# Kernel tuning notes

Hardware: AMD Instinct MI355X
Metric: run time of the kernel (lower is better)

The kernel has to match this reference:

```python
import jax, jax.numpy as jnp
import numpy as np

NUM_STUDENTS = 50000
NUM_PROBLEMS = 10000
EMBED_DIM = 64
NNZ = 3200000


def _spmm(rows, cols, vals, x, num_out):
    # out[r] = sum_{edges e with rows[e]==r} vals[e] * x[cols[e]]
    msgs = vals[:, None] * x[cols]  # [nnz, d]
    return jax.ops.segment_sum(msgs, rows, num_segments=num_out)


def setup_inputs() -> dict:
    key = jax.random.key(0)
    ks = jax.random.split(key, 8)
    return {
        "student_embeds": jax.random.normal(ks[0], (NUM_STUDENTS, EMBED_DIM), jnp.float32),
        "problem_embeds": jax.random.normal(ks[1], (NUM_PROBLEMS, EMBED_DIM), jnp.float32),
        "a_rows": jax.random.randint(ks[2], (NNZ,), 0, NUM_STUDENTS, jnp.int32),
        "a_cols": jax.random.randint(ks[3], (NNZ,), 0, NUM_PROBLEMS, jnp.int32),
        "a_vals": jax.random.uniform(ks[4], (NNZ,), jnp.float32),
        "ia_rows": jax.random.randint(ks[5], (NNZ,), 0, NUM_STUDENTS, jnp.int32),
        "ia_cols": jax.random.randint(ks[6], (NNZ,), 0, NUM_PROBLEMS, jnp.int32),
        "ia_vals": jax.random.uniform(ks[7], (NNZ,), jnp.float32),
    }


def reference(student_embeds, problem_embeds, a_rows, a_cols, a_vals,
              ia_rows, ia_cols, ia_vals):
    num_students = student_embeds.shape[0]
    num_problems = problem_embeds.shape[0]
    # a_matrix @ problem_embeds
    student_embeds_c = _spmm(a_rows, a_cols, a_vals, problem_embeds, num_students)
    # a_matrix.T @ student_embeds (swap roles of rows/cols)
    problem_embeds_c = _spmm(a_cols, a_rows, a_vals, student_embeds, num_problems)
    student_embeds_ic = _spmm(ia_rows, ia_cols, ia_vals, problem_embeds, num_students)
    problem_embeds_ic = _spmm(ia_cols, ia_rows, ia_vals, student_embeds, num_problems)
    return (student_embeds_c, student_embeds_ic, problem_embeds_c, problem_embeds_ic)
```

## Files before the change

### kernel.cpp

```cpp
#include <hip/hip_runtime.h>
#include <hip/hip_bf16.h>

#define NBMAX 256
#define TILE  4096
#define KPT   16
#define FTILE 2048
#define FKPT  8
#define BINSMAX 512

__device__ __forceinline__ int seg8(unsigned r, unsigned mult8) {
    return (int)__umulhi(r, mult8);
}

__global__ __launch_bounds__(256) void hist_all(
        const int* __restrict__ k0, const int* __restrict__ k1,
        const int* __restrict__ k2, const int* __restrict__ k3,
        int* __restrict__ gcnt4, int nnz, int rsh_s, int rsh_p) {
    __shared__ int h[NBMAX];
    int dir = blockIdx.x & 3;
    const int* key = (dir == 0) ? k0 : (dir == 1) ? k1 : (dir == 2) ? k2 : k3;
    int rsh = (dir & 1) ? rsh_p : rsh_s;
    h[threadIdx.x] = 0;
    __syncthreads();
    int ch = blockIdx.x >> 2, nch = gridDim.x >> 2;
    int nnz4 = nnz >> 2;
    for (int i = ch * 256 + threadIdx.x; i < nnz4; i += nch * 256) {
        int4 k4 = ((const int4*)key)[i];
        atomicAdd(&h[k4.x >> rsh], 1);
        atomicAdd(&h[k4.y >> rsh], 1);
        atomicAdd(&h[k4.z >> rsh], 1);
        atomicAdd(&h[k4.w >> rsh], 1);
    }
    if (ch == 0) {
        for (int i = (nnz4 << 2) + threadIdx.x; i < nnz; i += 256)
            atomicAdd(&h[key[i] >> rsh], 1);
    }
    __syncthreads();
    int v = h[threadIdx.x];
    if (v) atomicAdd(&gcnt4[dir * NBMAX + threadIdx.x], v);
}

__global__ __launch_bounds__(256) void scan_all(
        const int* __restrict__ gcnt4, int* __restrict__ boffs4,
        int* __restrict__ bcur4, int nb_s, int nb_p, int nnz,
        int* __restrict__ offsE, int* __restrict__ offsO, int NS, int NP8) {
    __shared__ int tmp[NBMAX];
    int dir = blockIdx.x, tid = threadIdx.x;
    int nb = (dir & 1) ? nb_p : nb_s;
    int v = (tid < nb) ? gcnt4[dir * NBMAX + tid] : 0;
    tmp[tid] = v;
    __syncthreads();
    for (int off = 1; off < NBMAX; off <<= 1) {
        int t = (tid >= off) ? tmp[tid - off] : 0;
        __syncthreads();
        tmp[tid] += t;
        __syncthreads();
    }
    if (tid < nb) {
        int e = tmp[tid] - v;
        boffs4[dir * (NBMAX + 1) + tid] = e;
        bcur4[dir * NBMAX + tid] = e;
    }
    if (tid == 0) boffs4[dir * (NBMAX + 1) + nb] = nnz;
    if (dir == 0 && tid == 0) { offsE[NS] = nnz; offsO[NP8] = nnz; }
}

__global__ __launch_bounds__(256) void staged_scatter(
        const int* __restrict__ key, const int* __restrict__ other,
        const float* __restrict__ vals, int* __restrict__ cursor,
        uint2* __restrict__ edges, int nnz, int rsh) {
    __shared__ int lhist[NBMAX], lofs[NBMAX], lbase[NBMAX];
    __shared__ uint2 stage[TILE];
    __shared__ int   sslot[TILE];
    int tid = threadIdx.x;
    int lmask = (1 << rsh) - 1;
    int ntiles = (nnz + TILE - 1) / TILE;
    for (int tile = blockIdx.x; tile < ntiles; tile += gridDim.x) {
        int tbeg = tile * TILE;
        int n = nnz - tbeg; if (n > TILE) n = TILE;
        lhist[tid] = 0;
        __syncthreads();
        int myb[KPT], myr[KPT]; unsigned myo[KPT]; float myv[KPT];
        #pragma unroll
        for (int g = 0; g < 4; ++g) {
            int s = g * 1024 + tid * 4;
            if (s + 4 <= n) {
                int i = tbeg + s;
                int4   k4 = *(const int4*)(key + i);
                int4   o4 = *(const int4*)(other + i);
                float4 v4 = *(const float4*)(vals + i);
                int   kk[4] = {k4.x, k4.y, k4.z, k4.w};
                int   oo[4] = {o4.x, o4.y, o4.z, o4.w};
                float vv[4] = {v4.x, v4.y, v4.z, v4.w};
                #pragma unroll
                for (int k = 0; k < 4; ++k) {
                    int m = g * 4 + k;
                    myb[m] = kk[k] >> rsh;
                    myo[m] = (unsigned)oo[k] | ((unsigned)(kk[k] & lmask) << 16);
                    myv[m] = vv[k];
                    myr[m] = atomicAdd(&lhist[myb[m]], 1);
                }
            } else {
                #pragma unroll
                for (int k = 0; k < 4; ++k) {
                    int m = g * 4 + k;
                    int s2 = s + k;
                    if (s2 < n) {
                        int i = tbeg + s2;
                        int ky = key[i];
                        myb[m] = ky >> rsh;
                        myo[m] = (unsigned)other[i] | ((unsigned)(ky & lmask) << 16);
                        myv[m] = vals[i];
                        myr[m] = atomicAdd(&lhist[myb[m]], 1);
                    } else myb[m] = -1;
                }
            }
        }
        __syncthreads();
        int h = lhist[tid];
        lofs[tid] = h;
        __syncthreads();
        for (int off = 1; off < NBMAX; off <<= 1) {
            int t = (tid >= off) ? lofs[tid - off] : 0;
            __syncthreads();
            lofs[tid] += t;
            __syncthreads();
        }
        lofs[tid] -= h;
        if (h > 0) lbase[tid] = atomicAdd(&cursor[tid], h);
        __syncthreads();
        #pragma unroll
        for (int k = 0; k < KPT; ++k) {
            if (myb[k] >= 0) {
                int ls = lofs[myb[k]] + myr[k];
                stage[ls] = make_uint2(myo[k], __float_as_uint(myv[k]));
                sslot[ls] = lbase[myb[k]] + myr[k];
            }
        }
        __syncthreads();
        #pragma unroll
        for (int k = 0; k < KPT; ++k) {
            int s = k * 256 + tid;
            if (s < n) edges[sslot[s]] = stage[s];
        }
        __syncthreads();
    }
}

__global__ __launch_bounds__(256) void staged_scatter2(
        const int* __restrict__ krow, const int* __restrict__ kcol,
        const float* __restrict__ vals,
        int* __restrict__ curE, int* __restrict__ curO,
        uint2* __restrict__ edgesE, uint2* __restrict__ edgesO,
        int nnz, int rsh_e, int rsh_o, int sgrid,
        const float* __restrict__ rpart, float* __restrict__ rout, int n4red) {
    __shared__ int lhistE[NBMAX], lofsE[NBMAX], lbaseE[NBMAX];
    __shared__ int lhistO[NBMAX], lofsO[NBMAX], lbaseO[NBMAX];
    __shared__ uint2 stageE[FTILE], stageO[FTILE];
    __shared__ int   sslotE[FTILE], sslotO[FTILE];
    int tid = threadIdx.x;
    int nred = (n4red + 255) >> 8;
    if ((int)blockIdx.x < nred) {
        int i = blockIdx.x * 256 + tid;
        if (i < n4red) {
            const float4* p = (const float4*)rpart;
            float4 s = make_float4(0.f, 0.f, 0.f, 0.f);
            #pragma unroll
            for (int xx = 0; xx < 8; ++xx) {
                float4 v = p[(size_t)xx * n4red + i];
                s.x += v.x; s.y += v.y; s.z += v.z; s.w += v.w;
            }
            ((float4*)rout)[i] = s;
        }
        return;
    }
    int sb = blockIdx.x - nred;
    int lmE = (1 << rsh_e) - 1, lmO = (1 << rsh_o) - 1;
    int ntiles = (nnz + FTILE - 1) / FTILE;
    for (int tile = sb; tile < ntiles; tile += sgrid) {
        int tbeg = tile * FTILE;
        int n = nnz - tbeg; if (n > FTILE) n = FTILE;
        lhistE[tid] = 0; lhistO[tid] = 0;
        __syncthreads();
        int mbE[FKPT], mrE[FKPT]; unsigned moE[FKPT];
        int mbO[FKPT], mrO[FKPT]; unsigned moO[FKPT];
        float mv[FKPT];
        #pragma unroll
        for (int g = 0; g < 2; ++g) {
            int s = g * 1024 + tid * 4;
            if (s + 4 <= n) {
                int i = tbeg + s;
                int4   r4 = *(const int4*)(krow + i);
                int4   c4 = *(const int4*)(kcol + i);
                float4 v4 = *(const float4*)(vals + i);
                int   rr[4] = {r4.x, r4.y, r4.z, r4.w};
                int   cc[4] = {c4.x, c4.y, c4.z, c4.w};
                float vv[4] = {v4.x, v4.y, v4.z, v4.w};
                #pragma unroll
                for (int k = 0; k < 4; ++k) {
                    int m = g * 4 + k;
                    mv[m]  = vv[k];
                    mbE[m] = rr[k] >> rsh_e;
                    moE[m] = (unsigned)cc[k] | ((unsigned)(rr[k] & lmE) << 16);
                    mrE[m] = atomicAdd(&lhistE[mbE[m]], 1);
                    mbO[m] = cc[k] >> rsh_o;
                    moO[m] = (unsigned)rr[k] | ((unsigned)(cc[k] & lmO) << 16);
                    mrO[m] = atomicAdd(&lhistO[mbO[m]], 1);
                }
            } else {
                #pragma unroll
                for (int k = 0; k < 4; ++k) {
                    int m = g * 4 + k;
                    int s2 = s + k;
                    if (s2 < n) {
                        int i = tbeg + s2;
                        int r = krow[i], c = kcol[i];
                        mv[m]  = vals[i];
                        mbE[m] = r >> rsh_e;
                        moE[m] = (unsigned)c | ((unsigned)(r & lmE) << 16);
                        mrE[m] = atomicAdd(&lhistE[mbE[m]], 1);
                        mbO[m] = c >> rsh_o;
                        moO[m] = (unsigned)r | ((unsigned)(c & lmO) << 16);
                        mrO[m] = atomicAdd(&lhistO[mbO[m]], 1);
                    } else { mbE[m] = -1; mbO[m] = -1; }
                }
            }
        }
        __syncthreads();
        int hE = lhistE[tid], hO = lhistO[tid];
        lofsE[tid] = hE; lofsO[tid] = hO;
        __syncthreads();
        for (int off = 1; off < NBMAX; off <<= 1) {
            int tE = (tid >= off) ? lofsE[tid - off] : 0;
            int tO = (tid >= off) ? lofsO[tid - off] : 0;
            __syncthreads();
            lofsE[tid] += tE; lofsO[tid] += tO;
            __syncthreads();
        }
        lofsE[tid] -= hE; lofsO[tid] -= hO;
        if (hE > 0) lbaseE[tid] = atomicAdd(&curE[tid], hE);
        if (hO > 0) lbaseO[tid] = atomicAdd(&curO[tid], hO);
        __syncthreads();
        #pragma unroll
        for (int k = 0; k < FKPT; ++k) {
            if (mbE[k] >= 0) {
                int lsE = lofsE[mbE[k]] + mrE[k];
                stageE[lsE] = make_uint2(moE[k], __float_as_uint(mv[k]));
                sslotE[lsE] = lbaseE[mbE[k]] + mrE[k];
                int lsO = lofsO[mbO[k]] + mrO[k];
                stageO[lsO] = make_uint2(moO[k], __float_as_uint(mv[k]));
                sslotO[lsO] = lbaseO[mbO[k]] + mrO[k];
            }
        }
        __syncthreads();
        #pragma unroll
        for (int k = 0; k < FKPT; ++k) {
            int s = k * 256 + tid;
            if (s < n) {
                edgesE[sslotE[s]] = stageE[s];
                edgesO[sslotO[s]] = stageO[s];
            }
        }
        __syncthreads();
    }
}

__global__ __launch_bounds__(512) void row_sort1(
        const uint2* __restrict__ e1, uint2* __restrict__ e2,
        const int* __restrict__ boffs, int* __restrict__ offs,
        int odd, int nb, int rsh, int nrows, unsigned mult8) {
    __shared__ int cnt[BINSMAX];
    __shared__ int tot[512];
    int tid = threadIdx.x;
    int b = blockIdx.x;
    if (b >= nb) return;
    int bins = odd ? (8 << rsh) : (1 << rsh);
    int beg = boffs[b], end = boffs[b + 1];
    if (tid < bins) cnt[tid] = 0;
    __syncthreads();
    for (int i = beg + tid; i < end; i += 512) {
        uint2 e = e1[i];
        int lrow = (int)(e.x >> 16);
        int bin = odd ? (lrow * 8 + seg8(e.x & 0xFFFFu, mult8)) : lrow;
        atomicAdd(&cnt[bin], 1);
    }
    __syncthreads();
    int own = (tid < bins) ? cnt[tid] : 0;
    tot[tid] = own;
    __syncthreads();
    for (int off = 1; off < 512; off <<= 1) {
        int t = (tid >= off) ? tot[tid - off] : 0;
        __syncthreads();
        tot[tid] += t;
        __syncthreads();
    }
    if (tid < bins) {
        int fineoff = tot[tid] - own;
        cnt[tid] = beg + fineoff;
        if (!odd) {
            int row = (b << rsh) + tid;
            if (row < nrows) offs[row] = beg + fineoff;
        } else {
            int row = (b << rsh) + (tid >> 3);
            if (row < nrows) offs[(row << 3) + (tid & 7)] = beg + fineoff;
        }
    }
    __syncthreads();
    for (int i = beg + tid; i < end; i += 512) {
        uint2 e = e1[i];
        int lrow = (int)(e.x >> 16);
        int bin = odd ? (lrow * 8 + seg8(e.x & 0xFFFFu, mult8)) : lrow;
        int slot = atomicAdd(&cnt[bin], 1);
        e2[slot] = make_uint2(e.x & 0xFFFFu, e.y);
    }
}

__device__ __forceinline__ void chunk_accum(
        float4& acc, uint2 e, int n, const float* __restrict__ xq, int q) {
    int   c0 = __shfl((int)e.x, q);
    float v0 = __uint_as_float(__shfl((int)e.y, q));
    int   c1 = __shfl((int)e.x, 4 + q);
    float v1 = __uint_as_float(__shfl((int)e.y, 4 + q));
    float4 x0 = *(const float4*)(xq + (((size_t)c0) << 6));
    float4 x1 = *(const float4*)(xq + (((size_t)c1) << 6));
    for (int j = 8; j < n; j += 8) {
        int   nc0 = __shfl((int)e.x, j + q);
        float nv0 = __uint_as_float(__shfl((int)e.y, j + q));
        int   nc1 = __shfl((int)e.x, j + 4 + q);
        float nv1 = __uint_as_float(__shfl((int)e.y, j + 4 + q));
        float4 nx0 = *(const float4*)(xq + (((size_t)nc0) << 6));
        float4 nx1 = *(const float4*)(xq + (((size_t)nc1) << 6));
        acc.x += v0 * x0.x; acc.y += v0 * x0.y;
        acc.z += v0 * x0.z; acc.w += v0 * x0.w;
        acc.x += v1 * x1.x; acc.y += v1 * x1.y;
        acc.z += v1 * x1.z; acc.w += v1 * x1.w;
        v0 = nv0; v1 = nv1; x0 = nx0; x1 = nx1;
    }
    acc.x += v0 * x0.x; acc.y += v0 * x0.y;
    acc.z += v0 * x0.z; acc.w += v0 * x0.w;
    acc.x += v1 * x1.x; acc.y += v1 * x1.y;
    acc.z += v1 * x1.z; acc.w += v1 * x1.w;
}

__device__ __forceinline__ float4 gather_pre(
        uint2 e0, int beg, int end, const uint2* __restrict__ edges,
        const float* __restrict__ xq, int q, int lane) {
    float4 acc = make_float4(0.f, 0.f, 0.f, 0.f);
    int n0 = end - beg; if (n0 > 64) n0 = 64;
    chunk_accum(acc, e0, n0, xq, q);
    for (int base = beg + 64; base < end; base += 64) {
        int n = end - base; if (n > 64) n = 64;
        uint2 e = make_uint2(0u, 0u);
        if (lane < n) e = edges[base + lane];
        chunk_accum(acc, e, n, xq, q);
    }
    acc.x += __shfl_xor(acc.x, 16); acc.y += __shfl_xor(acc.y, 16);
    acc.z += __shfl_xor(acc.z, 16); acc.w += __shfl_xor(acc.w, 16);
    acc.x += __shfl_xor(acc.x, 32); acc.y += __shfl_xor(acc.y, 32);
    acc.z += __shfl_xor(acc.z, 32); acc.w += __shfl_xor(acc.w, 32);
    return acc;
}

__device__ __forceinline__ void gatherE_body(
        int rA, const int* __restrict__ offs, const uint2* __restrict__ edges,
        const float* __restrict__ x, float* __restrict__ out, int nrows,
        int lane) {
    int q = lane >> 4, l16 = lane & 15;
    const float* xq = x + (l16 << 2);
    if (rA >= nrows) return;
    int rB = rA + 1;
    int begA = offs[rA], endA = offs[rA + 1];
    int begB = 0, endB = 0;
    if (rB < nrows) { begB = offs[rB]; endB = offs[rB + 1]; }
    int nA = endA - begA; if (nA > 64) nA = 64;
    int nB = endB - begB; if (nB > 64) nB = 64;
    uint2 eA = make_uint2(0u, 0u), eB = make_uint2(0u, 0u);
    if (lane < nA) eA = edges[begA + lane];
    if (lane < nB) eB = edges[begB + lane];
    float4 accA = gather_pre(eA, begA, endA, edges, xq, q, lane);
    if ((lane >> 4) == 0)
        *(float4*)(out + (((size_t)rA) << 6) + (l16 << 2)) = accA;
    if (rB < nrows) {
        float4 accB = gather_pre(eB, begB, endB, edges, xq, q, lane);
        if ((lane >> 4) == 0)
            *(float4*)(out + (((size_t)rB) << 6) + (l16 << 2)) = accB;
    }
}

__global__ __launch_bounds__(256) void row_gather(
        const int* __restrict__ offs, const uint2* __restrict__ edges,
        const float* __restrict__ x, float* __restrict__ out, int nrows) {
    int wave = threadIdx.x >> 6, lane = threadIdx.x & 63;
    gatherE_body(blockIdx.x * 8 + wave * 2, offs, edges, x, out, nrows, lane);
}

__global__ __launch_bounds__(512) void gatherE_sortO(
        const int* __restrict__ offsE_, const uint2* __restrict__ e2g,
        const float* __restrict__ xg, float* __restrict__ outg, int nrows,
        const uint2* __restrict__ e1s, uint2* __restrict__ e2s,
        const int* __restrict__ boffsS, int* __restrict__ offsS,
        int nb, int rsh, int nrowsS, unsigned mult8) {
    int tid = threadIdx.x;
    if ((int)blockIdx.x >= nb) {
        int gb = blockIdx.x - nb;
        int wave = tid >> 6, lane = tid & 63;
        gatherE_body(gb * 16 + wave * 2, offsE_, e2g, xg, outg, nrows, lane);
        return;
    }
    __shared__ int cnt[BINSMAX];
    __shared__ int tot[512];
    int b = blockIdx.x;
    int bins = 8 << rsh;
    int beg = boffsS[b], end = boffsS[b + 1];
    if (tid < bins) cnt[tid] = 0;
    __syncthreads();
    for (int i = beg + tid; i < end; i += 512) {
        uint2 e = e1s[i];
        int lrow = (int)(e.x >> 16);
        int bin = lrow * 8 + seg8(e.x & 0xFFFFu, mult8);
        atomicAdd(&cnt[bin], 1);
    }
    __syncthreads();
    int own = (tid < bins) ? cnt[tid] : 0;
    tot[tid] = own;
    __syncthreads();
    for (int off = 1; off < 512; off <<= 1) {
        int t = (tid >= off) ? tot[tid - off] : 0;
        __syncthreads();
        tot[tid] += t;
        __syncthreads();
    }
    if (tid < bins) {
        int fineoff = tot[tid] - own;
        cnt[tid] = beg + fineoff;
        int row = (b << rsh) + (tid >> 3);
        if (row < nrowsS) offsS[(row << 3) + (tid & 7)] = beg + fineoff;
    }
    __syncthreads();
    for (int i = beg + tid; i < end; i += 512) {
        uint2 e = e1s[i];
        int lrow = (int)(e.x >> 16);
        int bin = lrow * 8 + seg8(e.x & 0xFFFFu, mult8);
        int slot = atomicAdd(&cnt[bin], 1);
        e2s[slot] = make_uint2(e.x & 0xFFFFu, e.y);
    }
}

__global__ __launch_bounds__(256) void xcd_gather(
        const int* __restrict__ offs, const uint2* __restrict__ edges,
        const float* __restrict__ x, float* __restrict__ partial, int NP) {
    int g = blockIdx.x;
    int slot = g & 7;
    int t = g >> 3;
    int wave = threadIdx.x >> 6, lane = threadIdx.x & 63;
    int q = lane >> 4, l16 = lane & 15;
    const float* xq = x + (l16 << 2);
    int rA = t * 8 + wave * 2;
    if (rA >= NP) return;
    int rB = rA + 1;
    int binA = rA * 8 + slot;
    int begA = offs[binA], endA = offs[binA + 1];
    int begB = 0, endB = 0;
    if (rB < NP) { int binB = rB * 8 + slot; begB = offs[binB]; endB = offs[binB + 1]; }
    int nA = endA - begA; if (nA > 64) nA = 64;
    int nB = endB - begB; if (nB > 64) nB = 64;
    uint2 eA = make_uint2(0u, 0u), eB = make_uint2(0u, 0u);
    if (lane < nA) eA = edges[begA + lane];
    if (lane < nB) eB = edges[begB + lane];
    float4 accA = gather_pre(eA, begA, endA, edges, xq, q, lane);
    if ((lane >> 4) == 0)
        *(float4*)(partial + (size_t)slot * NP * 64 + (((size_t)rA) << 6) + (l16 << 2)) = accA;
    if (rB < NP) {
        float4 accB = gather_pre(eB, begB, endB, edges, xq, q, lane);
        if ((lane >> 4) == 0)
            *(float4*)(partial + (size_t)slot * NP * 64 + (((size_t)rB) << 6) + (l16 << 2)) = accB;
    }
}

__global__ __launch_bounds__(256) void reduce8(
        const float* __restrict__ partial, float* __restrict__ out, int n4) {
    int i = blockIdx.x * 256 + threadIdx.x;
    if (i < n4) {
        const float4* p = (const float4*)partial;
        float4 s = make_float4(0.f, 0.f, 0.f, 0.f);
        #pragma unroll
        for (int xx = 0; xx < 8; ++xx) {
            float4 v = p[(size_t)xx * n4 + i];
            s.x += v.x; s.y += v.y; s.z += v.z; s.w += v.w;
        }
        ((float4*)out)[i] = s;
    }
}

__global__ void spmm_scatter_kernel(const int* __restrict__ rows, const int* __restrict__ cols,
                                    const float* __restrict__ vals,
                                    const float* __restrict__ s_emb, const float* __restrict__ p_emb,
                                    float* __restrict__ out_s, float* __restrict__ out_p, int nnz) {
    long long t = (long long)blockIdx.x * blockDim.x + threadIdx.x;
    int e = (int)(t >> 6);
    int d = (int)(t & 63);
    if (e >= nnz) return;
    int r = rows[e];
    int c = cols[e];
    float v = vals[e];
    atomicAdd(&out_s[(size_t)r * 64 + d], v * p_emb[(size_t)c * 64 + d]);
    atomicAdd(&out_p[(size_t)c * 64 + d], v * s_emb[(size_t)r * 64 + d]);
}

extern "C" void kernel_launch(void* const* d_in, const int* in_sizes, int n_in,
                              void* d_out, int out_size, void* d_ws, size_t ws_size,
                              hipStream_t stream) {
    const float* s_emb   = (const float*)d_in[0];
    const float* p_emb   = (const float*)d_in[1];
    const int*   a_rows  = (const int*)d_in[2];
    const int*   a_cols  = (const int*)d_in[3];
    const float* a_vals  = (const float*)d_in[4];
    const int*   ia_rows = (const int*)d_in[5];
    const int*   ia_cols = (const int*)d_in[6];
    const float* ia_vals = (const float*)d_in[7];

    const int NS  = in_sizes[0] / 64;
    const int NP  = in_sizes[1] / 64;
    const int nnz = in_sizes[2];
    const int NP8 = NP * 8;

    float* out = (float*)d_out;
    float* out_sc  = out;
    float* out_sic = out_sc  + (size_t)NS * 64;
    float* out_pc  = out_sic + (size_t)NS * 64;
    float* out_pic = out_pc  + (size_t)NP * 64;

    int rsh_s = 0; while ((((long long)NS + (1LL << rsh_s) - 1) >> rsh_s) > NBMAX) rsh_s++;
    int rsh_p = 0; while ((((long long)NP + (1LL << rsh_p) - 1) >> rsh_p) > NBMAX) rsh_p++;
    int nb_s = (NS + (1 << rsh_s) - 1) >> rsh_s;
    int nb_p = (NP + (1 << rsh_p) - 1) >> rsh_p;
    unsigned mult8 = (unsigned)((8ULL << 32) / (unsigned)NS);

    const size_t edges_bytes = (size_t)nnz * sizeof(uint2);
    const size_t offsE_bytes = (size_t)(NS + 1) * sizeof(int);
    const size_t offsO_bytes = (size_t)(NP8 + 1) * sizeof(int);
    const size_t fixed_bytes = offsE_bytes + offsO_bytes
                      + (size_t)(4 * NBMAX + 4 * (NBMAX + 1) + 4 * NBMAX) * sizeof(int) + 256;
    const size_t need  = 2 * edges_bytes + fixed_bytes;
    const size_t need3 = 3 * edges_bytes + fixed_bytes;
    const bool packable = (NS <= 0xFFFF) && (NP <= 0xFFFF) &&
                          ((1 << rsh_s) <= BINSMAX) && ((8 << rsh_p) <= BINSMAX) &&
                          (edges_bytes >= (size_t)NP8 * 64 * sizeof(float)) &&
                          ((NP * 64) % 4 == 0);

    if (ws_size < need || !packable) {
        hipMemsetAsync(d_out, 0, (size_t)out_size * sizeof(float), stream);
        const long long total = (long long)nnz * 64;
        const int grid = (int)((total + 255) / 256);
        spmm_scatter_kernel<<<grid, 256, 0, stream>>>(a_rows, a_cols, a_vals, s_emb, p_emb,
                                                      out_sc, out_pc, nnz);
        spmm_scatter_kernel<<<grid, 256, 0, stream>>>(ia_rows, ia_cols, ia_vals, s_emb, p_emb,
                                                      out_sic, out_pic, nnz);
        return;
    }

    const bool fused = (ws_size >= need3);

    char* w = (char*)d_ws;
    uint2* edges1 = (uint2*)w;  w += edges_bytes;
    uint2* edges2 = (uint2*)w;  w += edges_bytes;
    uint2* edges3 = nullptr;
    if (fused) { edges3 = (uint2*)w; w += edges_bytes; }
    int*   offsE  = (int*)w;    w += offsE_bytes;
    int*   offsO  = (int*)w;    w += offsO_bytes;
    int*   gcnt4  = (int*)w;    w += 4 * NBMAX * sizeof(int);
    int*   boffs4 = (int*)w;    w += 4 * (NBMAX + 1) * sizeof(int);
    int*   bcur4  = (int*)w;

    hipMemsetAsync(gcnt4, 0, 4 * NBMAX * sizeof(int), stream);
    hist_all<<<1024, 256, 0, stream>>>(a_rows, a_cols, ia_rows, ia_cols,
                                       gcnt4, nnz, rsh_s, rsh_p);
    scan_all<<<4, 256, 0, stream>>>(gcnt4, boffs4, bcur4, nb_s, nb_p, nnz,
                                    offsE, offsO, NS, NP8);

    if (fused) {
        const int ntiles2 = (nnz + FTILE - 1) / FTILE;
        const int ggrid = (NS + 15) / 16;
        const int n4red = NP * 64 / 4;
        const int nred  = (n4red + 255) / 256;
        struct Mat { const int* r; const int* c; const float* v;
                     float* oe; float* oo; int de, dodd; };
        Mat mats[2] = {
            { a_rows,  a_cols,  a_vals,  out_sc,  out_pc,  0, 1 },
            { ia_rows, ia_cols, ia_vals, out_sic, out_pic, 2, 3 },
        };
        for (int m = 0; m < 2; ++m) {
            const Mat& M = mats[m];
            int red_n4 = (m == 1) ? n4red : 0;
            int red_blocks = (m == 1) ? nred : 0;
            staged_scatter2<<<ntiles2 + red_blocks, 256, 0, stream>>>(
                    M.r, M.c, M.v,
                    bcur4 + M.de * NBMAX, bcur4 + M.dodd * NBMAX,
                    edges1, edges3, nnz, rsh_s, rsh_p, ntiles2,
                    (const float*)edges2, mats[0].oo, red_n4);
            row_sort1<<<nb_s, 512, 0, stream>>>(edges1, edges2,
                    boffs4 + M.de * (NBMAX + 1), offsE, 0, nb_s, rsh_s, NS, mult8);
            gatherE_sortO<<<nb_p + ggrid, 512, 0, stream>>>(
                    offsE, edges2, p_emb, M.oe, NS,
                    edges3, edges1, boffs4 + M.dodd * (NBMAX + 1), offsO,
                    nb_p, rsh_p, NP, mult8);
            xcd_gather<<<8 * ((NP + 7) / 8), 256, 0, stream>>>(offsO, edges1,
                    s_emb, (float*)edges2, NP);
        }
        reduce8<<<(n4red + 255) / 256, 256, 0, stream>>>((const float*)edges2,
                mats[1].oo, n4red);
        return;
    }

    float* partial = (float*)edges1;
    const int ntiles = (nnz + TILE - 1) / TILE;
    struct Dir { const int* key; const int* other; const float* vals;
                 float* out; int odd; };
    Dir dirs[4] = {
        { a_rows,  a_cols,  a_vals,  out_sc,  0 },
        { a_cols,  a_rows,  a_vals,  out_pc,  1 },
        { ia_rows, ia_cols, ia_vals, out_sic, 0 },
        { ia_cols, ia_rows, ia_vals, out_pic, 1 },
    };
    for (int t = 0; t < 4; ++t) {
        const Dir& D = dirs[t];
        if (!D.odd) {
            staged_scatter<<<ntiles, 256, 0, stream>>>(D.key, D.other, D.vals,
                                                       bcur4 + t * NBMAX, edges1, nnz, rsh_s);
            row_sort1<<<nb_s, 512, 0, stream>>>(edges1, edges2,
                                                boffs4 + t * (NBMAX + 1), offsE,
                                                0, nb_s, rsh_s, NS, mult8);
            row_gather<<<(NS + 7) / 8, 256, 0, stream>>>(offsE, edges2, p_emb, D.out, NS);
        } else {
            staged_scatter<<<ntiles, 256, 0, stream>>>(D.key, D.other, D.vals,
                                                       bcur4 + t * NBMAX, edges1, nnz, rsh_p);
            row_sort1<<<nb_p, 512, 0, stream>>>(edges1, edges2,
                                                boffs4 + t * (NBMAX + 1), offsO,
                                                1, nb_p, rsh_p, NP, mult8);
            xcd_gather<<<8 * ((NP + 7) / 8), 256, 0, stream>>>(offsO, edges2,
                                                               s_emb, partial, NP);
            reduce8<<<(NP * 64 / 4 + 255) / 256, 256, 0, stream>>>(partial, D.out, NP * 64 / 4);
        }
    }
}
```

Measured before the change: 536.9 us.

## Interleave both matrices' sort and gather stages with five edge buffers

Adds a five-buffer path in which the second matrix's sort runs in the same launch as the first matrix's odd-direction gather, and the first matrix's partial reduction shares a launch with the second matrix's sort/gather. The sort and gather bodies are factored into device functions so they can be combined in these mixed kernels. The aim is to fill the GPU with independent work in each launch and to cut the number of launches and the tail idle time between dependent stages. It needs two more edge-sized workspace buffers and only takes effect if the workspace is large enough.

```diff
diff --git a/kernel.cpp b/kernel.cpp
--- a/kernel.cpp
+++ b/kernel.cpp
@@ -265,15 +265,12 @@
     }
 }
 
-__global__ __launch_bounds__(512) void row_sort1(
+__device__ __forceinline__ void sort_body(
         const uint2* __restrict__ e1, uint2* __restrict__ e2,
         const int* __restrict__ boffs, int* __restrict__ offs,
-        int odd, int nb, int rsh, int nrows, unsigned mult8) {
-    __shared__ int cnt[BINSMAX];
-    __shared__ int tot[512];
+        int odd, int b, int rsh, int nrows, unsigned mult8,
+        int* cnt, int* tot) {
     int tid = threadIdx.x;
-    int b = blockIdx.x;
-    if (b >= nb) return;
     int bins = odd ? (8 << rsh) : (1 << rsh);
     int beg = boffs[b], end = boffs[b + 1];
     if (tid < bins) cnt[tid] = 0;
@@ -313,6 +310,17 @@
         int slot = atomicAdd(&cnt[bin], 1);
         e2[slot] = make_uint2(e.x & 0xFFFFu, e.y);
     }
+}
+
+__global__ __launch_bounds__(512) void row_sort1(
+        const uint2* __restrict__ e1, uint2* __restrict__ e2,
+        const int* __restrict__ boffs, int* __restrict__ offs,
+        int odd, int nb, int rsh, int nrows, unsigned mult8) {
+    __shared__ int cnt[BINSMAX];
+    __shared__ int tot[512];
+    int b = blockIdx.x;
+    if (b >= nb) return;
+    sort_body(e1, e2, boffs, offs, odd, b, rsh, nrows, mult8, cnt, tot);
 }
 
 __device__ __forceinline__ void chunk_accum(
@@ -387,75 +395,12 @@
     }
 }
 
-__global__ __launch_bounds__(256) void row_gather(
-        const int* __restrict__ offs, const uint2* __restrict__ edges,
-        const float* __restrict__ x, float* __restrict__ out, int nrows) {
-    int wave = threadIdx.x >> 6, lane = threadIdx.x & 63;
-    gatherE_body(blockIdx.x * 8 + wave * 2, offs, edges, x, out, nrows, lane);
-}
-
-__global__ __launch_bounds__(512) void gatherE_sortO(
-        const int* __restrict__ offsE_, const uint2* __restrict__ e2g,
-        const float* __restrict__ xg, float* __restrict__ outg, int nrows,
-        const uint2* __restrict__ e1s, uint2* __restrict__ e2s,
-        const int* __restrict__ boffsS, int* __restrict__ offsS,
-        int nb, int rsh, int nrowsS, unsigned mult8) {
-    int tid = threadIdx.x;
-    if ((int)blockIdx.x >= nb) {
-        int gb = blockIdx.x - nb;
-        int wave = tid >> 6, lane = tid & 63;
-        gatherE_body(gb * 16 + wave * 2, offsE_, e2g, xg, outg, nrows, lane);
-        return;
-    }
-    __shared__ int cnt[BINSMAX];
-    __shared__ int tot[512];
-    int b = blockIdx.x;
-    int bins = 8 << rsh;
-    int beg = boffsS[b], end = boffsS[b + 1];
-    if (tid < bins) cnt[tid] = 0;
-    __syncthreads();
-    for (int i = beg + tid; i < end; i += 512) {
-        uint2 e = e1s[i];
-        int lrow = (int)(e.x >> 16);
-        int bin = lrow * 8 + seg8(e.x & 0xFFFFu, mult8);
-        atomicAdd(&cnt[bin], 1);
-    }
-    __syncthreads();
-    int own = (tid < bins) ? cnt[tid] : 0;
-    tot[tid] = own;
-    __syncthreads();
-    for (int off = 1; off < 512; off <<= 1) {
-        int t = (tid >= off) ? tot[tid - off] : 0;
-        __syncthreads();
-        tot[tid] += t;
-        __syncthreads();
-    }
-    if (tid < bins) {
-        int fineoff = tot[tid] - own;
-        cnt[tid] = beg + fineoff;
-        int row = (b << rsh) + (tid >> 3);
-        if (row < nrowsS) offsS[(row << 3) + (tid & 7)] = beg + fineoff;
-    }
-    __syncthreads();
-    for (int i = beg + tid; i < end; i += 512) {
-        uint2 e = e1s[i];
-        int lrow = (int)(e.x >> 16);
-        int bin = lrow * 8 + seg8(e.x & 0xFFFFu, mult8);
-        int slot = atomicAdd(&cnt[bin], 1);
-        e2s[slot] = make_uint2(e.x & 0xFFFFu, e.y);
-    }
-}
-
-__global__ __launch_bounds__(256) void xcd_gather(
-        const int* __restrict__ offs, const uint2* __restrict__ edges,
-        const float* __restrict__ x, float* __restrict__ partial, int NP) {
-    int g = blockIdx.x;
-    int slot = g & 7;
-    int t = g >> 3;
-    int wave = threadIdx.x >> 6, lane = threadIdx.x & 63;
+__device__ __forceinline__ void xcdO_body(
+        int rA, int slot, const int* __restrict__ offs,
+        const uint2* __restrict__ edges, const float* __restrict__ x,
+        float* __restrict__ partial, int NP, int lane) {
     int q = lane >> 4, l16 = lane & 15;
     const float* xq = x + (l16 << 2);
-    int rA = t * 8 + wave * 2;
     if (rA >= NP) return;
     int rB = rA + 1;
     int binA = rA * 8 + slot;
@@ -477,6 +422,77 @@
     }
 }
 
+__global__ __launch_bounds__(256) void row_gather(
+        const int* __restrict__ offs, const uint2* __restrict__ edges,
+        const float* __restrict__ x, float* __restrict__ out, int nrows) {
+    int wave = threadIdx.x >> 6, lane = threadIdx.x & 63;
+    gatherE_body(blockIdx.x * 8 + wave * 2, offs, edges, x, out, nrows, lane);
+}
+
+__global__ __launch_bounds__(512) void gatherE_sortO(
+        const int* __restrict__ offsE_, const uint2* __restrict__ e2g,
+        const float* __restrict__ xg, float* __restrict__ outg, int nrows,
+        const uint2* __restrict__ e1s, uint2* __restrict__ e2s,
+        const int* __restrict__ boffsS, int* __restrict__ offsS,
+        int nb, int rsh, int nrowsS, unsigned mult8,
+        const float* __restrict__ rpart, float* __restrict__ rout, int n4red) {
+    int tid = threadIdx.x;
+    int nred = (n4red + 511) >> 9;
+    if ((int)blockIdx.x >= nb + nred) {
+        int gb = blockIdx.x - nb - nred;
+        int wave = tid >> 6, lane = tid & 63;
+        gatherE_body(gb * 16 + wave * 2, offsE_, e2g, xg, outg, nrows, lane);
+        return;
+    }
+    if ((int)blockIdx.x >= nb) {
+        int i = (blockIdx.x - nb) * 512 + tid;
+        if (i < n4red) {
+            const float4* p = (const float4*)rpart;
+            float4 s = make_float4(0.f, 0.f, 0.f, 0.f);
+            #pragma unroll
+            for (int xx = 0; xx < 8; ++xx) {
+                float4 v = p[(size_t)xx * n4red + i];
+                s.x += v.x; s.y += v.y; s.z += v.z; s.w += v.w;
+            }
+            ((float4*)rout)[i] = s;
+        }
+        return;
+    }
+    __shared__ int cnt[BINSMAX];
+    __shared__ int tot[512];
+    sort_body(e1s, e2s, boffsS, offsS, 1, blockIdx.x, rsh, nrowsS, mult8, cnt, tot);
+}
+
+__global__ __launch_bounds__(512) void sortE_xcd(
+        const uint2* __restrict__ e_in, uint2* __restrict__ e_out,
+        const int* __restrict__ boffsS, int* __restrict__ offsS,
+        int nb, int rsh, int nrowsS, unsigned mult8,
+        const int* __restrict__ offsO, const uint2* __restrict__ edgesO,
+        const float* __restrict__ x, float* __restrict__ partial, int NP) {
+    int tid = threadIdx.x;
+    if ((int)blockIdx.x >= nb) {
+        int xg = blockIdx.x - nb;
+        int slot = xg & 7;
+        int t = xg >> 3;
+        int wave = tid >> 6, lane = tid & 63;
+        xcdO_body(t * 16 + wave * 2, slot, offsO, edgesO, x, partial, NP, lane);
+        return;
+    }
+    __shared__ int cnt[BINSMAX];
+    __shared__ int tot[512];
+    sort_body(e_in, e_out, boffsS, offsS, 0, blockIdx.x, rsh, nrowsS, mult8, cnt, tot);
+}
+
+__global__ __launch_bounds__(256) void xcd_gather(
+        const int* __restrict__ offs, const uint2* __restrict__ edges,
+        const float* __restrict__ x, float* __restrict__ partial, int NP) {
+    int g = blockIdx.x;
+    int slot = g & 7;
+    int t = g >> 3;
+    int wave = threadIdx.x >> 6, lane = threadIdx.x & 63;
+    xcdO_body(t * 8 + wave * 2, slot, offs, edges, x, partial, NP, lane);
+}
+
 __global__ __launch_bounds__(256) void reduce8(
         const float* __restrict__ partial, float* __restrict__ out, int n4) {
     int i = blockIdx.x * 256 + threadIdx.x;
@@ -543,6 +559,7 @@
                       + (size_t)(4 * NBMAX + 4 * (NBMAX + 1) + 4 * NBMAX) * sizeof(int) + 256;
     const size_t need  = 2 * edges_bytes + fixed_bytes;
     const size_t need3 = 3 * edges_bytes + fixed_bytes;
+    const size_t need5 = 5 * edges_bytes + fixed_bytes;
     const bool packable = (NS <= 0xFFFF) && (NP <= 0xFFFF) &&
                           ((1 << rsh_s) <= BINSMAX) && ((8 << rsh_p) <= BINSMAX) &&
                           (edges_bytes >= (size_t)NP8 * 64 * sizeof(float)) &&
@@ -559,13 +576,16 @@
         return;
     }
 
-    const bool fused = (ws_size >= need3);
+    const bool fused  = (ws_size >= need3);
+    const bool fused5 = (ws_size >= need5);
 
     char* w = (char*)d_ws;
     uint2* edges1 = (uint2*)w;  w += edges_bytes;
     uint2* edges2 = (uint2*)w;  w += edges_bytes;
-    uint2* edges3 = nullptr;
-    if (fused) { edges3 = (uint2*)w; w += edges_bytes; }
+    uint2* edges3 = nullptr; uint2* edges4 = nullptr; uint2* edges5 = nullptr;
+    if (fused)  { edges3 = (uint2*)w; w += edges_bytes; }
+    if (fused5) { edges4 = (uint2*)w; w += edges_bytes;
+                  edges5 = (uint2*)w; w += edges_bytes; }
     int*   offsE  = (int*)w;    w += offsE_bytes;
     int*   offsO  = (int*)w;    w += offsO_bytes;
     int*   gcnt4  = (int*)w;    w += 4 * NBMAX * sizeof(int);
@@ -578,11 +598,45 @@
     scan_all<<<4, 256, 0, stream>>>(gcnt4, boffs4, bcur4, nb_s, nb_p, nnz,
                                     offsE, offsO, NS, NP8);
 
+    const int ntiles2 = (nnz + FTILE - 1) / FTILE;
+    const int ggrid   = (NS + 15) / 16;
+    const int n4red   = NP * 64 / 4;
+    const int nredG   = (n4red + 511) / 512;
+
+    if (fused5) {
+        staged_scatter2<<<ntiles2, 256, 0, stream>>>(a_rows, a_cols, a_vals,
+                bcur4 + 0 * NBMAX, bcur4 + 1 * NBMAX,
+                edges1, edges2, nnz, rsh_s, rsh_p, ntiles2,
+                nullptr, nullptr, 0);
+        row_sort1<<<nb_s, 512, 0, stream>>>(edges1, edges3,
+                boffs4 + 0 * (NBMAX + 1), offsE, 0, nb_s, rsh_s, NS, mult8);
+        gatherE_sortO<<<nb_p + ggrid, 512, 0, stream>>>(
+                offsE, edges3, p_emb, out_sc, NS,
+                edges2, edges1, boffs4 + 1 * (NBMAX + 1), offsO,
+                nb_p, rsh_p, NP, mult8, nullptr, nullptr, 0);
+        staged_scatter2<<<ntiles2, 256, 0, stream>>>(ia_rows, ia_cols, ia_vals,
+                bcur4 + 2 * NBMAX, bcur4 + 3 * NBMAX,
+                edges2, edges4, nnz, rsh_s, rsh_p, ntiles2,
+                nullptr, nullptr, 0);
+        const int xgrid = 8 * ((NP + 15) / 16);
+        sortE_xcd<<<nb_s + xgrid, 512, 0, stream>>>(
+                edges2, edges3, boffs4 + 2 * (NBMAX + 1), offsE,
+                nb_s, rsh_s, NS, mult8,
+                offsO, edges1, s_emb, (float*)edges5, NP);
+        gatherE_sortO<<<nb_p + nredG + ggrid, 512, 0, stream>>>(
+                offsE, edges3, p_emb, out_sic, NS,
+                edges4, edges2, boffs4 + 3 * (NBMAX + 1), offsO,
+                nb_p, rsh_p, NP, mult8,
+                (const float*)edges5, out_pc, n4red);
+        xcd_gather<<<8 * ((NP + 7) / 8), 256, 0, stream>>>(offsO, edges2,
+                s_emb, (float*)edges1, NP);
+        reduce8<<<(n4red + 255) / 256, 256, 0, stream>>>((const float*)edges1,
+                out_pic, n4red);
+        return;
+    }
+
     if (fused) {
-        const int ntiles2 = (nnz + FTILE - 1) / FTILE;
-        const int ggrid = (NS + 15) / 16;
-        const int n4red = NP * 64 / 4;
-        const int nred  = (n4red + 255) / 256;
+        const int nred = (n4red + 255) / 256;
         struct Mat { const int* r; const int* c; const float* v;
                      float* oe; float* oo; int de, dodd; };
         Mat mats[2] = {
@@ -603,7 +657,7 @@
             gatherE_sortO<<<nb_p + ggrid, 512, 0, stream>>>(
                     offsE, edges2, p_emb, M.oe, NS,
                     edges3, edges1, boffs4 + M.dodd * (NBMAX + 1), offsO,
-                    nb_p, rsh_p, NP, mult8);
+                    nb_p, rsh_p, NP, mult8, nullptr, nullptr, 0);
             xcd_gather<<<8 * ((NP + 7) / 8), 256, 0, stream>>>(offsO, edges1,
                     s_emb, (float*)edges2, NP);
         }
```

Result: no change. 526.9 us (-1.9%).
